# Kernel optimization log

Measured on AMD Instinct MI355X. Metric: run time of the kernel, lower is better.

## Reference

```python
import jax, jax.numpy as jnp
import numpy as np

NE = 32          # n_events
S = 65536        # n_samples
FR = 128         # n_frames
SR = 22050       # samplerate
NRES = 1024      # n_resonances
IEXP = 8         # instr_expressivity
NEXP = 4         # noise_expressivity
NFILT = 64       # n_noise_filters
FSAMP = 512      # noise_filter_samples
NDEF = 64        # n_deformations
NNDEF = 32       # noise_deformations
NENV = 64        # n_envelopes
NDEC = 64        # n_decays
ENV_SMALL = 128  # Envelopes n_samples
ENV_FULL = 8192  # Envelopes full_size
NVERB = 16       # number of impulse responses


def interp_last(x, size):
    # linear interpolation along last axis (align_corners=True style)
    n = x.shape[-1]
    pos = jnp.linspace(0.0, n - 1.0, size)
    lo = jnp.floor(pos).astype(jnp.int32)
    hi = jnp.clip(lo + 1, 0, n - 1)
    w = (pos - lo).astype(x.dtype)
    return x[..., lo] * (1.0 - w) + x[..., hi] * w


def fft_convolve(a, b):
    # linear convolution via zero-padded FFT, keep first n samples
    n = a.shape[-1]
    A = jnp.fft.rfft(a, n=2 * n)
    B = jnp.fft.rfft(b, n=2 * n)
    return jnp.fft.irfft(A * B, n=2 * n)[..., :n]


def select_items(sel, items):
    # softmax-weighted soft lookup over item bank
    return jax.nn.softmax(sel, axis=-1) @ items


def make_waves(n_samples, n_res, sr):
    freqs = np.linspace(20.0, 4000.0, num=n_res // 4)
    t = np.arange(n_samples, dtype=np.float64) / sr
    ph = freqs[:, None] * t[None, :]               # cycles
    sine = np.sin(2 * np.pi * ph)
    saw = 2.0 * (ph % 1.0) - 1.0
    square = np.sign(sine)
    tri = 2.0 * np.abs(saw) - 1.0
    w = np.concatenate([sine, saw, square, tri], axis=0)  # (n_res, n_samples)
    return jnp.asarray(w, dtype=jnp.float32)


def setup_inputs() -> dict:
    key = jax.random.key(0)
    ks = jax.random.split(key, 16)
    u = lambda k, shp: jax.random.uniform(k, shp, minval=-0.02, maxval=0.02, dtype=jnp.float32)
    inp = {
        'res_sel': jax.random.normal(ks[0], (1, NE, IEXP, NRES), jnp.float32),
        'noise_sel': jax.random.normal(ks[1], (1, NE, NEXP, NFILT), jnp.float32),
        'env_sel': jax.random.normal(ks[2], (1, NE, NENV), jnp.float32),
        'dec_sel': jax.random.normal(ks[3], (1, NE, 1, NDEC), jnp.float32),
        'def_sel': jax.random.normal(ks[4], (1, NE, NDEF), jnp.float32),
        'noise_def_sel': jax.random.normal(ks[5], (1, NE, NNDEF), jnp.float32),
        'mix_sel': jax.random.normal(ks[6], (1, NE, 2), jnp.float32),
        'room_sel': jax.random.normal(ks[7], (1, NE, NVERB), jnp.float32),
        'amp': jax.random.uniform(ks[8], (1, NE, 1), dtype=jnp.float32),
        # learned item banks (uniform(-0.02, 0.02) init as in Lookup)
        'r_items': u(ks[9], (NRES, NRES)),
        'n_items': u(ks[10], (NFILT, FSAMP)),
        'e_items': u(ks[11], (NENV, ENV_SMALL)),
        'd_items': u(ks[12], (NDEC, 1)),
        'warp_items': u(ks[13], (NDEF, IEXP * FR)),
        'nwarp_items': u(ks[14], (NNDEF, NEXP * FR)),
        # fixed buffers
        'verbs': jax.random.normal(ks[15], (NVERB, S), jnp.float32) * 0.01,
        'waves': make_waves(S, NRES, SR),
    }
    return inp


def reference(res_sel, noise_sel, env_sel, dec_sel, def_sel, noise_def_sel,
              mix_sel, room_sel, amp, r_items, n_items, e_items, d_items,
              warp_items, nwarp_items, verbs, waves):
    # --- Envelopes: items**2, soft lookup, upsample, multiply by noise, pad ---
    env = select_items(env_sel, e_items ** 2)            # (1, NE, 128)
    env = interp_last(env, ENV_FULL)                     # (1, NE, 8192)
    noise = jax.random.uniform(jax.random.key(42), env.shape,
                               minval=-1.0, maxval=1.0, dtype=env.dtype)
    env = env * noise
    impulses = jnp.pad(env, ((0, 0), (0, 0), (0, S - ENV_FULL)))  # (1, NE, S)

    # --- SampleLookup (windowed noise filters) ---
    k = jnp.arange(FSAMP, dtype=jnp.float32)
    hamming = 0.54 - 0.46 * jnp.cos(2.0 * jnp.pi * k / (FSAMP - 1))
    nfil = select_items(noise_sel, n_items * hamming)    # (1, NE, NEXP, FSAMP)
    nfil = jnp.pad(nfil, ((0, 0), (0, 0), (0, 0), (0, S - FSAMP)))
    filt = fft_convolve(impulses[:, :, None, :], nfil)   # (1, NE, NEXP, S)

    # --- noise Deformations: softmax over channel dim, upsample ---
    nd = select_items(noise_def_sel, nwarp_items)        # (1, NE, NEXP*FR)
    nd = nd.reshape(1, NE, NEXP, FR)
    nd = jax.nn.softmax(nd, axis=2)
    nd = interp_last(nd, S)                              # (1, NE, NEXP, S)
    filtered = (filt * nd).sum(axis=2)                   # (1, NE, S)

    # --- WavetableLookup resonances ---
    res = select_items(res_sel, r_items) @ waves         # (1, NE, IEXP, S)

    # --- Decays: log-domain cumsum -> exponential envelopes ---
    d_pre = 0.5 + jax.nn.sigmoid(d_items) * 0.5          # base_resonance=0.5
    d = select_items(dec_sel, d_pre)                     # (1, NE, 1, 1)
    d = jnp.tile(d, (1, 1, 1, FR))                       # (1, NE, 1, FR)
    d = jnp.exp(jnp.cumsum(jnp.log(d + 1e-12), axis=-1))
    d = interp_last(d, S)                                # (1, NE, 1, S)

    # --- instrument Deformations ---
    w = select_items(def_sel, warp_items)                # (1, NE, IEXP*FR)
    w = w.reshape(1, NE, IEXP, FR)
    w = jax.nn.softmax(w, axis=2)
    w = interp_last(w, S)                                # (1, NE, IEXP, S)

    dres = (res * d * w).sum(axis=2)                     # (1, NE, S)

    # --- excite resonances with filtered noise, add reverb, mix ---
    conv = fft_convolve(filtered, dres)                  # (1, NE, S)
    rooms = select_items(room_sel, verbs)                # (1, NE, S)
    wet = fft_convolve(conv, rooms)
    m = jax.nn.softmax(mix_sel, axis=-1)                 # (1, NE, 2)
    mixed = m[..., 0:1] * conv + m[..., 1:2] * wet
    return mixed * (amp ** 2)                            # (1, NE, S)
```

## Files before the change

kernel.cpp:

```cpp
#include <hip/hip_runtime.h>
#include <math.h>

#define NEV    32
#define NS     65536
#define NFFT   131072
#define ENVS   128
#define ENVF   8192
#define FSAMP2 512
#define NEXP2  4
#define FLEN   8704
#define GD     5622750u
#define GDH    2811375u

enum : size_t {
  O_ENV_SMALL = 0,
  O_NFIL      = 4096,
  O_IMP       = 69632,
  O_ND        = 331776,
  O_WSM       = 348160,
  O_DSM       = 380928,
  O_SCAL      = 385024,
  O_RHO       = 385152,
  O_P1        = 385664,
  O_P2        = 647808,
  O_FILT      = 909952,
  O_DRES      = 1188480,
  O_CONV      = 3285632,
  O_ROOMS     = 5382784,
  O_SWE       = 7479936,
  O_SWN       = 7482048,
  O_SWD       = 7490304,
  O_SWND      = 7492416,
  O_X         = 7742080,
  O_Y         = 16130688,
  O_END       = 24519296,
};

typedef float f32x4 __attribute__((ext_vector_type(4)));
typedef short bf16x8 __attribute__((ext_vector_type(8)));

union U8 { uint4 q; bf16x8 v; unsigned short u[8]; };

__device__ __forceinline__ int imin(int a, int b){ return a < b ? a : b; }

__device__ __forceinline__ float wsum(float v){
  #pragma unroll
  for (int o = 32; o > 0; o >>= 1) v += __shfl_xor(v, o);
  return v;
}
__device__ __forceinline__ float wmax(float v){
  #pragma unroll
  for (int o = 32; o > 0; o >>= 1) v = fmaxf(v, __shfl_xor(v, o));
  return v;
}

__device__ __forceinline__ unsigned short f2bf(float f){
  unsigned u = __float_as_uint(f);
  unsigned r = (u + 0x7fffu + ((u >> 16) & 1u)) >> 16;
  return (unsigned short)r;
}

__device__ __forceinline__ float2 twid(float frac){
  float c, s;
  asm("v_cos_f32 %0, %1" : "=v"(c) : "v"(frac));
  asm("v_sin_f32 %0, %1" : "=v"(s) : "v"(frac));
  return make_float2(c, -s);
}

__device__ __forceinline__ unsigned tf_rotl(unsigned x, int d){ return (x << d) | (x >> (32 - d)); }

__device__ unsigned threefry_bits(unsigned chi, unsigned clo){
  const unsigned k0 = 0u, k1 = 42u, k2 = 0x1BD11BDAu ^ 0u ^ 42u;
  unsigned x0 = chi + k0;
  unsigned x1 = clo + k1;
  x0 += x1; x1 = tf_rotl(x1,13); x1 ^= x0;
  x0 += x1; x1 = tf_rotl(x1,15); x1 ^= x0;
  x0 += x1; x1 = tf_rotl(x1,26); x1 ^= x0;
  x0 += x1; x1 = tf_rotl(x1, 6); x1 ^= x0;
  x0 += k1; x1 += k2 + 1u;
  x0 += x1; x1 = tf_rotl(x1,17); x1 ^= x0;
  x0 += x1; x1 = tf_rotl(x1,29); x1 ^= x0;
  x0 += x1; x1 = tf_rotl(x1,16); x1 ^= x0;
  x0 += x1; x1 = tf_rotl(x1,24); x1 ^= x0;
  x0 += k2; x1 += k0 + 2u;
  x0 += x1; x1 = tf_rotl(x1,13); x1 ^= x0;
  x0 += x1; x1 = tf_rotl(x1,15); x1 ^= x0;
  x0 += x1; x1 = tf_rotl(x1,26); x1 ^= x0;
  x0 += x1; x1 = tf_rotl(x1, 6); x1 ^= x0;
  x0 += k0; x1 += k1 + 3u;
  x0 += x1; x1 = tf_rotl(x1,17); x1 ^= x0;
  x0 += x1; x1 = tf_rotl(x1,29); x1 ^= x0;
  x0 += x1; x1 = tf_rotl(x1,16); x1 ^= x0;
  x0 += x1; x1 = tf_rotl(x1,24); x1 ^= x0;
  x0 += k1; x1 += k2 + 4u;
  x0 += x1; x1 = tf_rotl(x1,13); x1 ^= x0;
  x0 += x1; x1 = tf_rotl(x1,15); x1 ^= x0;
  x0 += x1; x1 = tf_rotl(x1,26); x1 ^= x0;
  x0 += x1; x1 = tf_rotl(x1, 6); x1 ^= x0;
  x0 += k2; x1 += k0 + 5u;
  return x0 ^ x1;
}

__global__ __launch_bounds__(64) void weights_kernel(
    const float* __restrict__ noise_sel, const float* __restrict__ env_sel,
    const float* __restrict__ dec_sel,   const float* __restrict__ def_sel,
    const float* __restrict__ ndef_sel,  const float* __restrict__ mix_sel,
    const float* __restrict__ room_sel,  const float* __restrict__ amp,
    const float* __restrict__ d_items,
    float* __restrict__ swE, float* __restrict__ swN,
    float* __restrict__ swD, float* __restrict__ swND,
    float* __restrict__ d_small, float* __restrict__ scal,
    float* __restrict__ rho)
{
  const int e = blockIdx.x;
  const int l = threadIdx.x;

  {
    float x = env_sel[e*64 + l];
    float mx = wmax(x);
    float ex = expf(x - mx);
    float sm = wsum(ex);
    swE[e*64 + l] = ex / sm;
  }
  #pragma unroll
  for (int x4 = 0; x4 < NEXP2; x4++){
    float v = noise_sel[(e*NEXP2 + x4)*64 + l];
    float mxv = wmax(v);
    float exv = expf(v - mxv);
    float smv = wsum(exv);
    swN[(e*NEXP2 + x4)*64 + l] = exv / smv;
  }
  {
    float x = def_sel[e*64 + l];
    float mx = wmax(x);
    float ex = expf(x - mx);
    float sm = wsum(ex);
    swD[e*64 + l] = ex / sm;
  }
  {
    float x = (l < 32) ? ndef_sel[e*32 + l] : -1e30f;
    float mx = wmax(x);
    float ex = (l < 32) ? expf(x - mx) : 0.f;
    float sm = wsum(ex);
    if (l < 32) swND[e*32 + l] = ex / sm;
  }
  {
    float x = dec_sel[e*64 + l];
    float mx = wmax(x);
    float ex = expf(x - mx);
    float sm = wsum(ex);
    float wgt = ex / sm;
    float di = d_items[l];
    float dp = 0.5f + 0.5f*(1.0f/(1.0f + expf(-di)));
    float d0 = wsum(wgt*dp);
    float ld = logf(d0 + 1e-12f);
    #pragma unroll
    for (int c = 0; c < 2; c++){
      int f = l + 64*c;
      d_small[e*128 + f] = expf((float)(f+1)*ld);
    }
  }
  if (l == 0){
    float a = mix_sel[e*2 + 0], b = mix_sel[e*2 + 1];
    float mm = fmaxf(a, b);
    float ea = expf(a - mm), eb = expf(b - mm);
    float ss = ea + eb;
    scal[e*4 + 0] = ea/ss;
    scal[e*4 + 1] = eb/ss;
    float am = amp[e];
    scal[e*4 + 2] = am*am;
  }
  {
    float x = (l < 16) ? room_sel[e*16 + l] : -1e30f;
    float mx = wmax(x);
    float ex = (l < 16) ? expf(x - mx) : 0.f;
    float sm = wsum(ex);
    if (l < 16) rho[e*16 + l] = ex/sm;
  }
}

__global__ __launch_bounds__(128) void envs_kernel(
    const float* __restrict__ swE, const float* __restrict__ e_items,
    float* __restrict__ env_small)
{
  const int e = blockIdx.x, j = threadIdx.x;
  __shared__ float sw[64];
  if (j < 64) sw[j] = swE[e*64 + j];
  __syncthreads();
  float acc = 0.f;
  #pragma unroll 8
  for (int k = 0; k < 64; k++){ float it = e_items[k*ENVS + j]; acc += sw[k]*(it*it); }
  env_small[e*ENVS + j] = acc;
}

__global__ __launch_bounds__(256) void nfil_kernel(
    const float* __restrict__ swN, const float* __restrict__ n_items,
    float* __restrict__ nfil)
{
  const int b = blockIdx.x;
  const int tid = threadIdx.x;
  __shared__ float sw[64];
  if (tid < 64) sw[tid] = swN[b*64 + tid];
  __syncthreads();
  #pragma unroll
  for (int c = 0; c < 2; c++){
    int tau = tid + 256*c;
    float acc = 0.f;
    #pragma unroll 8
    for (int f = 0; f < 64; f++) acc += sw[f]*n_items[f*FSAMP2 + tau];
    float ham = 0.54f - 0.46f*cosf((6.2831853071795864769f * (float)tau) / 511.0f);
    nfil[b*FSAMP2 + tau] = acc*ham;
  }
}

__global__ __launch_bounds__(128) void warp_kernel(
    const float* __restrict__ swD, const float* __restrict__ warp_items,
    float* __restrict__ w_small)
{
  const int e = blockIdx.x, f = threadIdx.x;
  __shared__ float sw[64];
  if (f < 64) sw[f] = swD[e*64 + f];
  __syncthreads();
  float acc[8] = {0,0,0,0,0,0,0,0};
  for (int k = 0; k < 64; k++){
    float wk = sw[k];
    const float* row = warp_items + (size_t)k*1024 + f;
    #pragma unroll
    for (int i = 0; i < 8; i++) acc[i] += wk*row[i*128];
  }
  float mx = -1e30f;
  #pragma unroll
  for (int i = 0; i < 8; i++) mx = fmaxf(mx, acc[i]);
  float ev[8]; float s = 0.f;
  #pragma unroll
  for (int i = 0; i < 8; i++){ ev[i] = expf(acc[i] - mx); s += ev[i]; }
  #pragma unroll
  for (int i = 0; i < 8; i++) w_small[(e*8 + i)*128 + f] = ev[i]/s;
}

__global__ __launch_bounds__(128) void nwarp_kernel(
    const float* __restrict__ swND, const float* __restrict__ nwarp_items,
    float* __restrict__ nd_small)
{
  const int e = blockIdx.x, f = threadIdx.x;
  __shared__ float sw[32];
  if (f < 32) sw[f] = swND[e*32 + f];
  __syncthreads();
  float acc[4] = {0,0,0,0};
  for (int k = 0; k < 32; k++){
    float wk = sw[k];
    const float* row = nwarp_items + (size_t)k*512 + f;
    #pragma unroll
    for (int x = 0; x < 4; x++) acc[x] += wk*row[x*128];
  }
  float mx = -1e30f;
  #pragma unroll
  for (int x = 0; x < 4; x++) mx = fmaxf(mx, acc[x]);
  float ev[4]; float s = 0.f;
  #pragma unroll
  for (int x = 0; x < 4; x++){ ev[x] = expf(acc[x] - mx); s += ev[x]; }
  #pragma unroll
  for (int x = 0; x < 4; x++) nd_small[(e*4 + x)*128 + f] = ev[x]/s;
}

__global__ __launch_bounds__(64) void prep_kernel(
    const float* __restrict__ noise_sel, const float* __restrict__ env_sel,
    const float* __restrict__ dec_sel,   const float* __restrict__ def_sel,
    const float* __restrict__ ndef_sel,  const float* __restrict__ mix_sel,
    const float* __restrict__ room_sel,  const float* __restrict__ amp,
    const float* __restrict__ n_items,   const float* __restrict__ e_items,
    const float* __restrict__ d_items,   const float* __restrict__ warp_items,
    const float* __restrict__ nwarp_items,
    float* __restrict__ env_small, float* __restrict__ nfil,
    float* __restrict__ nd_small,  float* __restrict__ w_small,
    float* __restrict__ d_small,   float* __restrict__ scal,
    float* __restrict__ rho)
{
  const int e = blockIdx.x;
  const int l = threadIdx.x;
  __shared__ float sw[64];
  __shared__ float buf[1024];

  {
    float x = env_sel[e*64 + l];
    float mx = wmax(x);
    float ex = expf(x - mx);
    float sm = wsum(ex);
    sw[l] = ex / sm;
  }
  __syncthreads();
  #pragma unroll
  for (int c = 0; c < 2; c++){
    int j = l + 64*c;
    float acc = 0.f;
    for (int k = 0; k < 64; k++){ float it = e_items[k*ENVS + j]; acc += sw[k]*(it*it); }
    env_small[e*ENVS + j] = acc;
  }
  __syncthreads();

  for (int x = 0; x < NEXP2; x++){
    float v = noise_sel[(e*NEXP2 + x)*64 + l];
    float mxv = wmax(v);
    float exv = expf(v - mxv);
    float smv = wsum(exv);
    sw[l] = exv / smv;
    __syncthreads();
    for (int c = 0; c < 8; c++){
      int tau = l + 64*c;
      float acc = 0.f;
      for (int f = 0; f < 64; f++) acc += sw[f]*n_items[f*FSAMP2 + tau];
      float ham = 0.54f - 0.46f*cosf((6.2831853071795864769f * (float)tau) / 511.0f);
      nfil[(e*NEXP2 + x)*FSAMP2 + tau] = acc*ham;
    }
    __syncthreads();
  }

  {
    float x = def_sel[e*64 + l];
    float mx = wmax(x);
    float ex = expf(x - mx);
    float sm = wsum(ex);
    sw[l] = ex / sm;
  }
  __syncthreads();
  for (int c = 0; c < 16; c++){
    int idx = l + 64*c;
    float acc = 0.f;
    for (int k = 0; k < 64; k++) acc += sw[k]*warp_items[k*1024 + idx];
    buf[idx] = acc;
  }
  __syncthreads();
  #pragma unroll
  for (int c = 0; c < 2; c++){
    int f = l + 64*c;
    float mx = -1e30f;
    for (int i = 0; i < 8; i++) mx = fmaxf(mx, buf[i*128 + f]);
    float ev[8]; float s = 0.f;
    for (int i = 0; i < 8; i++){ ev[i] = expf(buf[i*128 + f] - mx); s += ev[i]; }
    for (int i = 0; i < 8; i++) w_small[(e*8 + i)*128 + f] = ev[i]/s;
  }
  __syncthreads();

  {
    float x = (l < 32) ? ndef_sel[e*32 + l] : -1e30f;
    float mx = wmax(x);
    float ex = (l < 32) ? expf(x - mx) : 0.f;
    float sm = wsum(ex);
    sw[l] = (l < 32) ? ex/sm : 0.f;
  }
  __syncthreads();
  for (int c = 0; c < 8; c++){
    int idx = l + 64*c;
    float acc = 0.f;
    for (int k = 0; k < 32; k++) acc += sw[k]*nwarp_items[k*512 + idx];
    buf[idx] = acc;
  }
  __syncthreads();
  #pragma unroll
  for (int c = 0; c < 2; c++){
    int j = l + 64*c;
    float mx = -1e30f;
    for (int x = 0; x < 4; x++) mx = fmaxf(mx, buf[x*128 + j]);
    float ev[4]; float s = 0.f;
    for (int x = 0; x < 4; x++){ ev[x] = expf(buf[x*128 + j] - mx); s += ev[x]; }
    for (int x = 0; x < 4; x++) nd_small[(e*4 + x)*128 + j] = ev[x]/s;
  }
  __syncthreads();

  {
    float x = dec_sel[e*64 + l];
    float mx = wmax(x);
    float ex = expf(x - mx);
    float sm = wsum(ex);
    float wgt = ex / sm;
    float di = d_items[l];
    float dp = 0.5f + 0.5f*(1.0f/(1.0f + expf(-di)));
    float d0 = wsum(wgt*dp);
    float ld = logf(d0 + 1e-12f);
    #pragma unroll
    for (int c = 0; c < 2; c++){
      int f = l + 64*c;
      d_small[e*128 + f] = expf((float)(f+1)*ld);
    }
  }
  if (l == 0){
    float a = mix_sel[e*2 + 0], b = mix_sel[e*2 + 1];
    float mm = fmaxf(a, b);
    float ea = expf(a - mm), eb = expf(b - mm);
    float ss = ea + eb;
    scal[e*4 + 0] = ea/ss;
    scal[e*4 + 1] = eb/ss;
    float am = amp[e];
    scal[e*4 + 2] = am*am;
  }
  {
    float x = (l < 16) ? room_sel[e*16 + l] : -1e30f;
    float mx = wmax(x);
    float ex = (l < 16) ? expf(x - mx) : 0.f;
    float sm = wsum(ex);
    if (l < 16) rho[e*16 + l] = ex/sm;
  }
}

__global__ __launch_bounds__(256) void p1_softmax_kernel(
    const float* __restrict__ res_sel, float* __restrict__ P1)
{
  const int m = blockIdx.x;
  const int tid = threadIdx.x;
  __shared__ float red[4], red2[4];
  const float* row = res_sel + (size_t)m*1024;
  float4 v = ((const float4*)row)[tid];
  float mx = fmaxf(fmaxf(v.x, v.y), fmaxf(v.z, v.w));
  #pragma unroll
  for (int o = 32; o > 0; o >>= 1) mx = fmaxf(mx, __shfl_xor(mx, o));
  if ((tid & 63) == 0) red[tid >> 6] = mx;
  __syncthreads();
  mx = fmaxf(fmaxf(red[0], red[1]), fmaxf(red[2], red[3]));
  float e0 = expf(v.x - mx), e1 = expf(v.y - mx), e2 = expf(v.z - mx), e3 = expf(v.w - mx);
  float s = e0 + e1 + e2 + e3;
  #pragma unroll
  for (int o = 32; o > 0; o >>= 1) s += __shfl_xor(s, o);
  if ((tid & 63) == 0) red2[tid >> 6] = s;
  __syncthreads();
  s = red2[0] + red2[1] + red2[2] + red2[3];
  float inv = 1.0f/s;
  ((float4*)(P1 + (size_t)m*1024))[tid] = make_float4(e0*inv, e1*inv, e2*inv, e3*inv);
}

__global__ __launch_bounds__(256) void p2_kernel(
    const float* __restrict__ P1, const float* __restrict__ r_items,
    float* __restrict__ P2)
{
  __shared__ __align__(16) float sp1[8][1024];
  const int bx = blockIdx.x;
  const int mg = blockIdx.y;
  const int tid = threadIdx.x;
  for (int idx = tid; idx < 2048; idx += 256)
    ((float4*)&sp1[0][0])[idx] = ((const float4*)(P1 + (size_t)mg*8*1024))[idx];
  __syncthreads();
  const int n = bx*256 + tid;
  float acc[8] = {0,0,0,0,0,0,0,0};
  for (int k = 0; k < 1024; k++){
    float wv = r_items[(size_t)k*1024 + n];
    #pragma unroll
    for (int r = 0; r < 8; r++) acc[r] += sp1[r][k]*wv;
  }
  #pragma unroll
  for (int r = 0; r < 8; r++) P2[(size_t)(mg*8 + r)*1024 + n] = acc[r];
}

__global__ __launch_bounds__(256) void split_a_kernel(
    const float* __restrict__ P2, unsigned short* __restrict__ Ahi)
{
  const int row = blockIdx.x;
  for (int k = threadIdx.x; k < 1024; k += 256){
    float f = P2[(size_t)row*1024 + k];
    Ahi[(size_t)(k >> 3)*2048 + row*8 + (k & 7)] = f2bf(f);
  }
}

__global__ __launch_bounds__(256) void env_noise_kernel(
    const float* __restrict__ env_small, float* __restrict__ impulses)
{
  const int flat = blockIdx.x*256 + threadIdx.x;
  const int e = flat >> 13, i = flat & 8191;
  unsigned bits = threefry_bits(0u, (unsigned)flat);
  float u01 = __uint_as_float((bits >> 9) | 0x3f800000u) - 1.0f;
  float nz  = fmaxf(-1.0f, u01*2.0f - 1.0f);
  float pos = (float)i * (127.0f/8191.0f);
  int lo = (int)floorf(pos);
  int hi = imin(lo + 1, 127);
  float w = pos - (float)lo;
  const float* es = env_small + e*ENVS;
  float v = es[lo]*(1.0f - w) + es[hi]*w;
  impulses[flat] = v*nz;
}

__global__ __launch_bounds__(256) void filt_kernel(
    const float* __restrict__ nfil, const float* __restrict__ impulses,
    const float* __restrict__ nd_small, float* __restrict__ filtered)
{
  __shared__ float nf[4*512];
  __shared__ float imp[768];
  const int e = blockIdx.y, t0 = blockIdx.x*256, tid = threadIdx.x;
  for (int idx = tid; idx < 2048; idx += 256) nf[idx] = nfil[e*2048 + idx];
  for (int idx = tid; idx < 768; idx += 256){
    int g = t0 - 512 + idx;
    imp[idx] = (g >= 0 && g < ENVF) ? impulses[e*ENVF + g] : 0.f;
  }
  __syncthreads();
  const int t = t0 + tid;
  float s0 = 0.f, s1 = 0.f, s2 = 0.f, s3 = 0.f;
  for (int tau = 0; tau < 512; tau++){
    float iv = imp[512 + tid - tau];
    s0 += nf[0*512 + tau]*iv;
    s1 += nf[1*512 + tau]*iv;
    s2 += nf[2*512 + tau]*iv;
    s3 += nf[3*512 + tau]*iv;
  }
  float pos = (float)t * (127.0f/65535.0f);
  int lo = (int)floorf(pos);
  int hi = imin(lo + 1, 127);
  float w = pos - (float)lo;
  const float* nds = nd_small + e*512;
  float acc = 0.f;
  acc += s0*(nds[0*128 + lo]*(1.0f - w) + nds[0*128 + hi]*w);
  acc += s1*(nds[1*128 + lo]*(1.0f - w) + nds[1*128 + hi]*w);
  acc += s2*(nds[2*128 + lo]*(1.0f - w) + nds[2*128 + hi]*w);
  acc += s3*(nds[3*128 + lo]*(1.0f - w) + nds[3*128 + hi]*w);
  filtered[e*FLEN + t] = acc;
}

__global__ __launch_bounds__(256) void rooms_kernel(
    const float* __restrict__ verbs, const float* __restrict__ rho,
    float* __restrict__ rooms)
{
  const int t = blockIdx.x*256 + threadIdx.x;
  const int e = blockIdx.y;
  float acc = 0.f;
  #pragma unroll
  for (int v = 0; v < 16; v++) acc += rho[e*16 + v]*verbs[(size_t)v*NS + t];
  rooms[(size_t)e*NS + t] = acc;
}

__device__ __noinline__ float slow_wave(int wf, int n, int i){
  const double stp = 3980.0 / 255.0;
  double fi = (i == 255) ? 4000.0 : __dadd_rn(__dmul_rn((double)i, stp), 20.0);
  double tn = (double)n / 22050.0;
  double ph = __dmul_rn(fi, tn);
  double fr = ph - trunc(ph);
  if (wf == 1) return (float)(2.0*fr - 1.0);
  if (wf == 3){ double sw = 2.0*fr - 1.0; return (float)(2.0*fabs(sw) - 1.0); }
  if (fr == 0.0 || fr == 0.5){
    if (ph == 0.0) return 0.0f;
    double sv = sin(__dmul_rn(6.283185307179586, ph));
    return (sv > 0.0) ? 1.0f : ((sv < 0.0) ? -1.0f : 0.0f);
  }
  return (fr < 0.5) ? 1.0f : -1.0f;
}

__device__ __forceinline__ void gen8(int wf, int n, int i0,
                                     unsigned m_in, unsigned stepn,
                                     U8& bh, U8& bl)
{
  unsigned m = m_in;
  #pragma unroll
  for (int j = 0; j < 8; j++){
    float fr = (float)m * (1.0f/5622750.0f);
    float val;
    bool rare;
    if (wf == 0){
      asm("v_sin_f32 %0, %1" : "=v"(val) : "v"(fr));
      rare = false;
    } else if (wf == 1){
      val = fmaf(fr, 2.0f, -1.0f);
      rare = (m == 0u);
    } else if (wf == 2){
      val = (m < GDH) ? 1.0f : -1.0f;
      rare = (m == 0u) || (m == GDH);
    } else {
      val = fmaf(fabsf(fmaf(fr, 2.0f, -1.0f)), 2.0f, -1.0f);
      rare = (m == 0u);
    }
    if (rare) val = slow_wave(wf, n, i0 + j);
    unsigned ub = __float_as_uint(val);
    unsigned th = ub & 0xFFFF0000u;
    float lres = val - __uint_as_float(th);
    bh.u[j] = (unsigned short)(ub >> 16);
    bl.u[j] = (unsigned short)(__float_as_uint(lres) >> 16);
    m += stepn;
    if (m >= GD) m -= GD;
  }
}

__global__ __launch_bounds__(512, 2) void gemm_dres_gen3_kernel(
    const unsigned short* __restrict__ Ahi,
    const float* __restrict__ w_small, const float* __restrict__ d_small,
    float* __restrict__ dres)
{
  __shared__ __align__(16) unsigned short Abuf[2][8192];

  const int tid = threadIdx.x;
  const int l = tid & 63, w = tid >> 6;
  const int g = l >> 4, c = l & 15;
  const int n = blockIdx.x*128 + w*16 + c;

  f32x4 acc[16];
  #pragma unroll
  for (int m = 0; m < 16; m++) acc[m] = (f32x4){0.f,0.f,0.f,0.f};

  const unsigned stepn = (3980u*(unsigned)n) % GD;
  const unsigned s32 = (32u*stepn) % GD;
  const unsigned K0g = 3980u*(unsigned)(g*8) + 5100u;
  const unsigned m0 = (unsigned)(((unsigned long long)(unsigned)n * K0g) % GD);
  unsigned mseg = m0;

  typedef const __attribute__((address_space(1))) void GV;
  typedef __attribute__((address_space(3))) void LV;

  #pragma unroll
  for (int q = 0; q < 2; q++){
    const unsigned short* src = Ahi + (size_t)q*4096 + (size_t)w*512 + (size_t)l*8;
    __builtin_amdgcn_global_load_lds((GV*)src, (LV*)&Abuf[0][q*4096 + w*512], 16, 0, 0);
  }
  __syncthreads();

  for (int k0 = 0; k0 < 1024; k0 += 32){
    const int cur = (k0 >> 5) & 1, nxt = cur ^ 1;
    const int wf = k0 >> 8;
    if ((k0 & 255) == 0) mseg = m0;

    if (k0 + 32 < 1024){
      const size_t slice = (size_t)((k0 + 32) >> 5) * 8192;
      #pragma unroll
      for (int q = 0; q < 2; q++){
        const unsigned short* src = Ahi + slice + (size_t)q*4096 + (size_t)w*512 + (size_t)l*8;
        __builtin_amdgcn_global_load_lds((GV*)src, (LV*)&Abuf[nxt][q*4096 + w*512], 16, 0, 0);
      }
    }

    const int i0 = (k0 & 255) + g*8;
    U8 bh, bl;
    gen8(wf, n, i0, mseg, stepn, bh, bl);
    mseg += s32; if (mseg >= GD) mseg -= GD;

    #pragma unroll
    for (int m = 0; m < 16; m++){
      U8 ah;
      ah.q = *(const uint4*)&Abuf[cur][g*2048 + (m*16 + c)*8];
      acc[m] = __builtin_amdgcn_mfma_f32_16x16x32_bf16(ah.v, bh.v, acc[m], 0, 0, 0);
      acc[m] = __builtin_amdgcn_mfma_f32_16x16x32_bf16(ah.v, bl.v, acc[m], 0, 0, 0);
    }
    __syncthreads();
  }

  const int t = n;
  float pos = (float)t * (127.0f/65535.0f);
  int lo = (int)floorf(pos);
  int hi = imin(lo + 1, 127);
  float fr = pos - (float)lo;
  #pragma unroll
  for (int m = 0; m < 16; m++){
    int e = 2*m + (g >> 1);
    float s = 0.f;
    #pragma unroll
    for (int jj = 0; jj < 4; jj++){
      int i = (g & 1)*4 + jj;
      const float* wr = w_small + (size_t)(e*8 + i)*128;
      float wi = wr[lo]*(1.0f - fr) + wr[hi]*fr;
      s += wi * acc[m][jj];
    }
    s += __shfl_xor(s, 16);
    if ((g & 1) == 0){
      float de = d_small[e*128 + lo]*(1.0f - fr) + d_small[e*128 + hi]*fr;
      dres[(size_t)e*NS + t] = de * s;
    }
  }
}

__global__ __launch_bounds__(256) void gemm_dres_kernel(
    const float* __restrict__ P2, const float* __restrict__ waves,
    const float* __restrict__ w_small, const float* __restrict__ d_small,
    float* __restrict__ dres)
{
  __shared__ __align__(16) float At[32][256];
  __shared__ __align__(16) float Bt[32][64];
  const int tid = threadIdx.x;
  const int tx = tid & 15, ty = tid >> 4;
  const int n0 = blockIdx.x * 64;
  float acc[16][4];
  #pragma unroll
  for (int a = 0; a < 16; a++)
    #pragma unroll
    for (int b = 0; b < 4; b++) acc[a][b] = 0.f;

  for (int k0 = 0; k0 < 1024; k0 += 32){
    {
      const float4* src = (const float4*)(P2 + (size_t)tid*1024 + k0);
      #pragma unroll
      for (int q = 0; q < 8; q++){
        float4 v = src[q];
        At[q*4 + 0][tid] = v.x; At[q*4 + 1][tid] = v.y;
        At[q*4 + 2][tid] = v.z; At[q*4 + 3][tid] = v.w;
      }
    }
    {
      int c  = tid & 15;
      int kr = tid >> 4;
      *(float4*)&Bt[kr][c*4]      = *((const float4*)(waves + (size_t)(k0 + kr)*NS + n0) + c);
      *(float4*)&Bt[kr + 16][c*4] = *((const float4*)(waves + (size_t)(k0 + kr + 16)*NS + n0) + c);
    }
    __syncthreads();
    #pragma unroll 4
    for (int k = 0; k < 32; k++){
      float a[16];
      *(float4*)&a[0]  = *(const float4*)&At[k][ty*16 + 0];
      *(float4*)&a[4]  = *(const float4*)&At[k][ty*16 + 4];
      *(float4*)&a[8]  = *(const float4*)&At[k][ty*16 + 8];
      *(float4*)&a[12] = *(const float4*)&At[k][ty*16 + 12];
      float4 b = *(const float4*)&Bt[k][tx*4];
      #pragma unroll
      for (int mi = 0; mi < 16; mi++){
        acc[mi][0] += a[mi]*b.x;
        acc[mi][1] += a[mi]*b.y;
        acc[mi][2] += a[mi]*b.z;
        acc[mi][3] += a[mi]*b.w;
      }
    }
    __syncthreads();
  }

  #pragma unroll
  for (int ni = 0; ni < 4; ni++){
    int t = n0 + tx*4 + ni;
    float pos = (float)t * (127.0f/65535.0f);
    int lo = (int)floorf(pos);
    int hi = imin(lo + 1, 127);
    float w = pos - (float)lo;
    #pragma unroll
    for (int ev2 = 0; ev2 < 2; ev2++){
      int e = ty*2 + ev2;
      float de = d_small[e*128 + lo]*(1.0f - w) + d_small[e*128 + hi]*w;
      float s = 0.f;
      #pragma unroll
      for (int i = 0; i < 8; i++){
        const float* wrow = w_small + (size_t)(e*8 + i)*128;
        float wi = wrow[lo]*(1.0f - w) + wrow[hi]*w;
        s += wi * acc[ev2*8 + i][ni];
      }
      dres[(size_t)e*NS + t] = de * s;
    }
  }
}


template<int L, int LOG2L, int DIR>
__device__ __forceinline__ void fft_core(float*& ra, float*& ia, float*& rb, float*& ib)
{
  __shared__ float2 stw[256];
  const int tid = threadIdx.x;
  stw[tid] = twid((float)tid * (1.0f/512.0f));
  #pragma unroll
  for (int s = 0; s < LOG2L; s++){
    const int Ns = 1 << s;
    __syncthreads();
    #pragma unroll
    for (int q = 0; q < 8; q++){
      int bf = tid + 256*q;
      int r  = bf >> (LOG2L - 1);
      int j  = bf & (L/2 - 1);
      int sw = (r & 7) << 2;
      int jm = j & (Ns - 1);
      float2 w = stw[jm << (8 - s)];
      float wi = (DIR > 0) ? w.y : -w.y;
      float a_re = ra[r*L + (j ^ sw)];
      float a_im = ia[r*L + (j ^ sw)];
      float b_re = ra[r*L + ((j + L/2) ^ sw)];
      float b_im = ia[r*L + ((j + L/2) ^ sw)];
      float t_re = b_re*w.x - b_im*wi;
      float t_im = b_re*wi + b_im*w.x;
      int d = ((j >> s) << (s + 1)) | jm;
      rb[r*L + (d ^ sw)]        = a_re + t_re;
      ib[r*L + (d ^ sw)]        = a_im + t_im;
      rb[r*L + ((d + Ns) ^ sw)] = a_re - t_re;
      ib[r*L + ((d + Ns) ^ sw)] = a_im - t_im;
    }
    float* t;
    t = ra; ra = rb; rb = t;
    t = ia; ia = ib; ib = t;
  }
  __syncthreads();
}

__global__ __launch_bounds__(256) void fwd512_pack_kernel(
    const float* __restrict__ srcA, int lenA, int strideA,
    const float* __restrict__ srcB, int lenB, int strideB,
    float2* __restrict__ Bt)
{
  __shared__ float reA[4096], imA[4096], reB[4096], imB[4096];
  const int e = blockIdx.y, t1 = blockIdx.x*8, tid = threadIdx.x;
  #pragma unroll
  for (int q = 0; q < 4; q++){
    int flat = tid + 256*q;
    int n2 = flat >> 1;
    int rb = (flat & 1)*4;
    int nb = t1 + rb + 256*n2;
    float4 va = make_float4(0.f,0.f,0.f,0.f);
    float4 vb = make_float4(0.f,0.f,0.f,0.f);
    if (nb < lenA) va = *(const float4*)(srcA + (size_t)e*strideA + nb);
    if (nb < lenB) vb = *(const float4*)(srcB + (size_t)e*strideB + nb);
    #pragma unroll
    for (int j = 0; j < 4; j++){
      int r = rb + j;
      int sw = (r & 7) << 2;
      reA[r*512 + (n2 ^ sw)] = (&va.x)[j];
      imA[r*512 + (n2 ^ sw)] = (&vb.x)[j];
    }
  }
  float *ra = reA, *ia = imA, *rb2 = reB, *ib2 = imB;
  fft_core<512, 9, +1>(ra, ia, rb2, ib2);
  float2* dst = Bt + ((size_t)e << 17);
  #pragma unroll
  for (int q = 0; q < 16; q++){
    int idx = tid + 256*q;
    int r = idx & 7, k2 = idx >> 3;
    int n1 = t1 + r;
    int sw = (r & 7) << 2;
    float xr = ra[r*512 + (k2 ^ sw)];
    float xi = ia[r*512 + (k2 ^ sw)];
    float2 w = twid((float)(n1*k2) * (1.0f/131072.0f));
    dst[k2*256 + n1] = make_float2(xr*w.x - xi*w.y, xr*w.y + xi*w.x);
  }
}

__global__ __launch_bounds__(256) void fwd512_pack_rooms_kernel(
    const float* __restrict__ verbs, const float* __restrict__ rho,
    float2* __restrict__ Bt)
{
  __shared__ float reA[4096], imA[4096], reB[4096], imB[4096];
  __shared__ float srho[32];
  const int e = blockIdx.y, t1 = blockIdx.x*8, tid = threadIdx.x;
  if (tid < 32) srho[tid] = rho[(2*e)*16 + tid];
  __syncthreads();
  #pragma unroll
  for (int q = 0; q < 4; q++){
    int flat = tid + 256*q;
    int n2 = flat >> 1;
    int rb = (flat & 1)*4;
    int nb = t1 + rb + 256*n2;
    float4 va = make_float4(0.f,0.f,0.f,0.f);
    float4 vb = make_float4(0.f,0.f,0.f,0.f);
    if (nb < NS){
      #pragma unroll
      for (int v = 0; v < 16; v++){
        float4 w4 = *(const float4*)(verbs + (size_t)v*NS + nb);
        float r0 = srho[v], r1 = srho[16 + v];
        va.x += r0*w4.x; va.y += r0*w4.y; va.z += r0*w4.z; va.w += r0*w4.w;
        vb.x += r1*w4.x; vb.y += r1*w4.y; vb.z += r1*w4.z; vb.w += r1*w4.w;
      }
    }
    #pragma unroll
    for (int j = 0; j < 4; j++){
      int r = rb + j;
      int sw = (r & 7) << 2;
      reA[r*512 + (n2 ^ sw)] = (&va.x)[j];
      imA[r*512 + (n2 ^ sw)] = (&vb.x)[j];
    }
  }
  float *ra = reA, *ia = imA, *rb2 = reB, *ib2 = imB;
  fft_core<512, 9, +1>(ra, ia, rb2, ib2);
  float2* dst = Bt + ((size_t)e << 17);
  #pragma unroll
  for (int q = 0; q < 16; q++){
    int idx = tid + 256*q;
    int r = idx & 7, k2 = idx >> 3;
    int n1 = t1 + r;
    int sw = (r & 7) << 2;
    float xr = ra[r*512 + (k2 ^ sw)];
    float xi = ia[r*512 + (k2 ^ sw)];
    float2 w = twid((float)(n1*k2) * (1.0f/131072.0f));
    dst[k2*256 + n1] = make_float2(xr*w.x - xi*w.y, xr*w.y + xi*w.x);
  }
}

__global__ __launch_bounds__(256) void fwd256_kernel(float2* __restrict__ S)
{
  __shared__ float reA[4096], imA[4096], reB[4096], imB[4096];
  const int e = blockIdx.y, K0 = blockIdx.x*16, tid = threadIdx.x;
  float2* base = S + ((size_t)e << 17) + (size_t)K0*256;
  #pragma unroll
  for (int q = 0; q < 16; q++){
    int idx = tid + 256*q;
    int r = idx >> 8, col = idx & 255;
    float2 v = base[r*256 + col];
    int sw = (r & 7) << 2;
    reA[r*256 + (col ^ sw)] = v.x;
    imA[r*256 + (col ^ sw)] = v.y;
  }
  float *ra = reA, *ia = imA, *rb = reB, *ib = imB;
  fft_core<256, 8, +1>(ra, ia, rb, ib);
  #pragma unroll
  for (int q = 0; q < 16; q++){
    int idx = tid + 256*q;
    int r = idx >> 8, col = idx & 255;
    int sw = (r & 7) << 2;
    base[r*256 + col] = make_float2(ra[r*256 + (col ^ sw)], ia[r*256 + (col ^ sw)]);
  }
}

__global__ __launch_bounds__(256) void inv256_mul2_kernel(
    const float2* __restrict__ ZA, const float2* __restrict__ ZB,
    float2* __restrict__ Ut)
{
  __shared__ float reA[4096], imA[4096], reB[4096], imB[4096];
  const int e = blockIdx.y, K0 = blockIdx.x*16, tid = threadIdx.x;
  const float2* Za = ZA + ((size_t)e << 17);
  const float2* Zb = ZB + ((size_t)e << 17);
  #pragma unroll
  for (int q = 0; q < 16; q++){
    int idx = tid + 256*q;
    int r = idx >> 8, col = idx & 255;
    int k2 = K0 + r;
    int k2p, k1p;
    if (k2 == 0){ k2p = 0; k1p = (256 - col) & 255; }
    else        { k2p = 512 - k2; k1p = 255 - col; }
    float2 za  = Za[(size_t)k2*256 + col];
    float2 zap = Za[(size_t)k2p*256 + k1p];
    float2 zb  = Zb[(size_t)k2*256 + col];
    float2 zbp = Zb[(size_t)k2p*256 + k1p];
    float a0r = 0.5f*(za.x + zap.x), a0i = 0.5f*(za.y - zap.y);
    float a1r = 0.5f*(za.y + zap.y), a1i = 0.5f*(zap.x - za.x);
    float b0r = 0.5f*(zb.x + zbp.x), b0i = 0.5f*(zb.y - zbp.y);
    float b1r = 0.5f*(zb.y + zbp.y), b1i = 0.5f*(zbp.x - zb.x);
    float p0r = a0r*b0r - a0i*b0i, p0i = a0r*b0i + a0i*b0r;
    float p1r = a1r*b1r - a1i*b1i, p1i = a1r*b1i + a1i*b1r;
    int sw = (r & 7) << 2;
    reA[r*256 + (col ^ sw)] = p0r - p1i;
    imA[r*256 + (col ^ sw)] = p0i + p1r;
  }
  float *ra = reA, *ia = imA, *rb = reB, *ib = imB;
  fft_core<256, 8, -1>(ra, ia, rb, ib);
  float2* dst = Ut + ((size_t)e << 17);
  #pragma unroll
  for (int q = 0; q < 16; q++){
    int idx = tid + 256*q;
    int r = idx & 15, n1 = idx >> 4;
    int k2 = K0 + r;
    int sw = (r & 7) << 2;
    float xr = ra[r*256 + (n1 ^ sw)];
    float xi = ia[r*256 + (n1 ^ sw)];
    float2 w = twid((float)(n1*k2) * (1.0f/131072.0f));
    dst[n1*512 + k2] = make_float2(xr*w.x + xi*w.y, xi*w.x - xr*w.y);
  }
}

__global__ __launch_bounds__(256) void inv512_fwdpack2_kernel(
    const float2* __restrict__ Ut, float* __restrict__ conv,
    float2* __restrict__ Bt)
{
  __shared__ float reA[4096], imA[4096], reB[4096], imB[4096];
  const int e = blockIdx.y, t1 = blockIdx.x*8, tid = threadIdx.x;
  const float2* base = Ut + ((size_t)e << 17) + (size_t)t1*512;
  #pragma unroll
  for (int q = 0; q < 16; q++){
    int idx = tid + 256*q;
    int r = idx >> 9, col = idx & 511;
    float2 v = base[r*512 + col];
    int sw = (r & 7) << 2;
    reA[r*512 + (col ^ sw)] = v.x;
    imA[r*512 + (col ^ sw)] = v.y;
  }
  float *ra = reA, *ia = imA, *rb = reB, *ib = imB;
  fft_core<512, 9, -1>(ra, ia, rb, ib);
  const float s = 1.0f/131072.0f;
  #pragma unroll
  for (int q = 0; q < 16; q++){
    int idx = tid + 256*q;
    int r = idx & 7, n2 = idx >> 3;
    int sw = (r & 7) << 2;
    int pos = r*512 + (n2 ^ sw);
    if (n2 < 256){
      int n = (t1 + r) + 256*n2;
      float y0 = ra[pos]*s, y1 = ia[pos]*s;
      conv[(size_t)(2*e)*NS + n]     = y0;
      conv[(size_t)(2*e + 1)*NS + n] = y1;
      rb[pos] = y0; ib[pos] = y1;
    } else {
      rb[pos] = 0.f; ib[pos] = 0.f;
    }
  }
  __syncthreads();
  float *r2 = rb, *i2 = ib, *r3 = ra, *i3 = ia;
  fft_core<512, 9, +1>(r2, i2, r3, i3);
  float2* dst = Bt + ((size_t)e << 17);
  #pragma unroll
  for (int q = 0; q < 16; q++){
    int idx = tid + 256*q;
    int r = idx & 7, k2 = idx >> 3;
    int n1 = t1 + r;
    int sw = (r & 7) << 2;
    float xr = r2[r*512 + (k2 ^ sw)];
    float xi = i2[r*512 + (k2 ^ sw)];
    float2 w = twid((float)(n1*k2) * (1.0f/131072.0f));
    dst[k2*256 + n1] = make_float2(xr*w.x - xi*w.y, xr*w.y + xi*w.x);
  }
}

__global__ __launch_bounds__(256) void inv512_mix2_kernel(
    const float2* __restrict__ Ut, const float* __restrict__ conv,
    const float* __restrict__ scal, float* __restrict__ dst)
{
  __shared__ float reA[4096], imA[4096], reB[4096], imB[4096];
  const int e = blockIdx.y, t1 = blockIdx.x*8, tid = threadIdx.x;
  const float2* base = Ut + ((size_t)e << 17) + (size_t)t1*512;
  #pragma unroll
  for (int q = 0; q < 16; q++){
    int idx = tid + 256*q;
    int r = idx >> 9, col = idx & 511;
    float2 v = base[r*512 + col];
    int sw = (r & 7) << 2;
    reA[r*512 + (col ^ sw)] = v.x;
    imA[r*512 + (col ^ sw)] = v.y;
  }
  float *ra = reA, *ia = imA, *rb = reB, *ib = imB;
  fft_core<512, 9, -1>(ra, ia, rb, ib);
  const float s = 1.0f/131072.0f;
  const int e0 = 2*e, e1 = 2*e + 1;
  float m00 = scal[e0*4 + 0], m10 = scal[e0*4 + 1], a20 = scal[e0*4 + 2];
  float m01 = scal[e1*4 + 0], m11 = scal[e1*4 + 1], a21 = scal[e1*4 + 2];
  #pragma unroll
  for (int q = 0; q < 8; q++){
    int idx = tid + 256*q;
    int r = idx & 7, n2 = idx >> 3;
    int n = (t1 + r) + 256*n2;
    int sw = (r & 7) << 2;
    int pos = r*512 + (n2 ^ sw);
    float w0 = ra[pos]*s, w1 = ia[pos]*s;
    size_t g0 = (size_t)e0*NS + n, g1 = (size_t)e1*NS + n;
    dst[g0] = (m00*conv[g0] + m10*w0)*a20;
    dst[g1] = (m01*conv[g1] + m11*w1)*a21;
  }
}

template<int MODE>
__global__ __launch_bounds__(256) void tconv_kernel(
    const float* __restrict__ sig, int sig_len, int sig_stride,
    const float* __restrict__ go, const float* __restrict__ scal,
    float* __restrict__ dst)
{
  __shared__ __align__(16) float cs[2048];
  __shared__ __align__(16) float rs[4104];
  const int e = blockIdx.y;
  const int t0 = blockIdx.x * 2048;
  const int tid = threadIdx.x;
  const int tb = tid * 8;
  float acc[8] = {0,0,0,0,0,0,0,0};
  const int kcap = imin(sig_len, t0 + 2048);
  for (int c0 = 0; c0 < kcap; c0 += 2048){
    __syncthreads();
    for (int idx = tid; idx < 2048; idx += 256){
      int gsi = c0 + idx;
      cs[idx] = (gsi < sig_len) ? sig[(size_t)e*sig_stride + gsi] : 0.f;
    }
    const int rb = t0 - c0 - 2056;
    for (int idx = tid; idx < 4104; idx += 256){
      int g = rb + idx;
      rs[idx] = (g >= 0 && g < NS) ? go[(size_t)e*NS + g] : 0.f;
    }
    __syncthreads();
    float W[12];
    int P = tb + 2056;
    *(float4*)&W[0] = *(const float4*)&rs[P - 4];
    *(float4*)&W[4] = *(const float4*)&rs[P];
    *(float4*)&W[8] = *(const float4*)&rs[P + 4];
    for (int u = 0; u < 512; u++){
      float4 f4 = *(const float4*)&cs[4*u];
      #pragma unroll
      for (int j = 0; j < 8; j++){
        acc[j] += f4.x*W[4 + j];
        acc[j] += f4.y*W[3 + j];
        acc[j] += f4.z*W[2 + j];
        acc[j] += f4.w*W[1 + j];
      }
      #pragma unroll
      for (int x2 = 11; x2 >= 4; x2--) W[x2] = W[x2 - 4];
      P -= 4;
      *(float4*)&W[0] = *(const float4*)&rs[P - 4];
    }
  }
  if (MODE == 0){
    #pragma unroll
    for (int j = 0; j < 8; j++) dst[(size_t)e*NS + t0 + tb + j] = acc[j];
  } else {
    float m0 = scal[e*4 + 0], m1 = scal[e*4 + 1], a2 = scal[e*4 + 2];
    #pragma unroll
    for (int j = 0; j < 8; j++){
      size_t gi = (size_t)e*NS + t0 + tb + j;
      dst[gi] = (m0*sig[gi] + m1*acc[j]) * a2;
    }
  }
}

extern "C" void kernel_launch(void* const* d_in, const int* in_sizes, int n_in,
                              void* d_out, int out_size, void* d_ws, size_t ws_size,
                              hipStream_t stream)
{
  (void)in_sizes; (void)n_in; (void)out_size;
  const float* res_sel     = (const float*)d_in[0];
  const float* noise_sel   = (const float*)d_in[1];
  const float* env_sel     = (const float*)d_in[2];
  const float* dec_sel     = (const float*)d_in[3];
  const float* def_sel     = (const float*)d_in[4];
  const float* ndef_sel    = (const float*)d_in[5];
  const float* mix_sel     = (const float*)d_in[6];
  const float* room_sel    = (const float*)d_in[7];
  const float* amp         = (const float*)d_in[8];
  const float* r_items     = (const float*)d_in[9];
  const float* n_items     = (const float*)d_in[10];
  const float* e_items     = (const float*)d_in[11];
  const float* d_items     = (const float*)d_in[12];
  const float* warp_items  = (const float*)d_in[13];
  const float* nwarp_items = (const float*)d_in[14];
  const float* verbs       = (const float*)d_in[15];
  const float* waves       = (const float*)d_in[16];
  float* ws  = (float*)d_ws;
  float* out = (float*)d_out;

  const bool big_ws = ws_size >= (size_t)O_END * sizeof(float);

  if (big_ws) {
    weights_kernel<<<dim3(NEV), dim3(64), 0, stream>>>(
        noise_sel, env_sel, dec_sel, def_sel, ndef_sel, mix_sel, room_sel, amp,
        d_items, ws + O_SWE, ws + O_SWN, ws + O_SWD, ws + O_SWND,
        ws + O_DSM, ws + O_SCAL, ws + O_RHO);
    envs_kernel<<<dim3(NEV), dim3(128), 0, stream>>>(ws + O_SWE, e_items, ws + O_ENV_SMALL);
    nfil_kernel<<<dim3(128), dim3(256), 0, stream>>>(ws + O_SWN, n_items, ws + O_NFIL);
    warp_kernel<<<dim3(NEV), dim3(128), 0, stream>>>(ws + O_SWD, warp_items, ws + O_WSM);
    nwarp_kernel<<<dim3(NEV), dim3(128), 0, stream>>>(ws + O_SWND, nwarp_items, ws + O_ND);

    p1_softmax_kernel<<<dim3(256), dim3(256), 0, stream>>>(res_sel, ws + O_P1);
    p2_kernel<<<dim3(4, 32), dim3(256), 0, stream>>>(ws + O_P1, r_items, ws + O_P2);

    env_noise_kernel<<<dim3(1024), dim3(256), 0, stream>>>(ws + O_ENV_SMALL, ws + O_IMP);
    filt_kernel<<<dim3(34, NEV), dim3(256), 0, stream>>>(ws + O_NFIL, ws + O_IMP, ws + O_ND, ws + O_FILT);

    unsigned short* Ahi = (unsigned short*)(ws + O_X);
    split_a_kernel<<<dim3(256), dim3(256), 0, stream>>>(ws + O_P2, Ahi);
    gemm_dres_gen3_kernel<<<dim3(512), dim3(512), 0, stream>>>(
        Ahi, ws + O_WSM, ws + O_DSM, ws + O_DRES);

    float2* Xf = (float2*)(ws + O_X);
    float2* Xd = (float2*)(ws + O_X + 4194304);
    float2* Xr = (float2*)(ws + O_Y);
    float2* Uc = (float2*)(ws + O_Y + 4194304);
    float2* Xc = Xf;
    float2* Uw = Xd;

    fwd512_pack_kernel<<<dim3(32, 16), dim3(256), 0, stream>>>(
        ws + O_FILT, FLEN, 2*FLEN, ws + O_FILT + FLEN, FLEN, 2*FLEN, Xf);
    fwd256_kernel<<<dim3(32, 16), dim3(256), 0, stream>>>(Xf);
    fwd512_pack_kernel<<<dim3(32, 16), dim3(256), 0, stream>>>(
        ws + O_DRES, NS, 2*NS, ws + O_DRES + NS, NS, 2*NS, Xd);
    fwd256_kernel<<<dim3(32, 16), dim3(256), 0, stream>>>(Xd);
    fwd512_pack_rooms_kernel<<<dim3(32, 16), dim3(256), 0, stream>>>(
        verbs, ws + O_RHO, Xr);
    fwd256_kernel<<<dim3(32, 16), dim3(256), 0, stream>>>(Xr);

    inv256_mul2_kernel<<<dim3(32, 16), dim3(256), 0, stream>>>(Xf, Xd, Uc);
    inv512_fwdpack2_kernel<<<dim3(32, 16), dim3(256), 0, stream>>>(Uc, ws + O_CONV, Xc);
    fwd256_kernel<<<dim3(32, 16), dim3(256), 0, stream>>>(Xc);
    inv256_mul2_kernel<<<dim3(32, 16), dim3(256), 0, stream>>>(Xc, Xr, Uw);
    inv512_mix2_kernel<<<dim3(32, 16), dim3(256), 0, stream>>>(
        Uw, ws + O_CONV, ws + O_SCAL, out);
  } else {
    prep_kernel<<<dim3(NEV), dim3(64), 0, stream>>>(
        noise_sel, env_sel, dec_sel, def_sel, ndef_sel, mix_sel, room_sel, amp,
        n_items, e_items, d_items, warp_items, nwarp_items,
        ws + O_ENV_SMALL, ws + O_NFIL, ws + O_ND, ws + O_WSM,
        ws + O_DSM, ws + O_SCAL, ws + O_RHO);
    p1_softmax_kernel<<<dim3(256), dim3(256), 0, stream>>>(res_sel, ws + O_P1);
    p2_kernel<<<dim3(4, 32), dim3(256), 0, stream>>>(ws + O_P1, r_items, ws + O_P2);
    env_noise_kernel<<<dim3(1024), dim3(256), 0, stream>>>(ws + O_ENV_SMALL, ws + O_IMP);
    filt_kernel<<<dim3(34, NEV), dim3(256), 0, stream>>>(ws + O_NFIL, ws + O_IMP, ws + O_ND, ws + O_FILT);
    rooms_kernel<<<dim3(256, NEV), dim3(256), 0, stream>>>(verbs, ws + O_RHO, ws + O_ROOMS);
    gemm_dres_kernel<<<dim3(1024), dim3(256), 0, stream>>>(
        ws + O_P2, waves, ws + O_WSM, ws + O_DSM, ws + O_DRES);
    tconv_kernel<0><<<dim3(32, NEV), dim3(256), 0, stream>>>(
        ws + O_FILT, FLEN, FLEN, ws + O_DRES, (const float*)nullptr, ws + O_CONV);
    tconv_kernel<1><<<dim3(32, NEV), dim3(256), 0, stream>>>(
        ws + O_CONV, NS, NS, ws + O_ROOMS, ws + O_SCAL, out);
  }
}
```

Before: 413.4 us.

## Replace radix-2 shared-memory FFT stages with radix-4 butterflies

Replaces the radix-2 Stockham FFT core used by all the 512- and 256-point passes with a radix-4 version (one radix-2 stage plus four radix-4 stages for L=512, four radix-4 stages for L=256). This roughly halves the number of LDS read/write passes and __syncthreads barriers per FFT. Twiddles are now computed per butterfly via twid() plus complex squaring instead of a shared lookup table, which adds ALU work and slight rounding differences.

Result: faster. 388.2 us (-6.1%).

```diff
diff --git a/kernel.cpp b/kernel.cpp
--- a/kernel.cpp
+++ b/kernel.cpp
@@ -734,40 +734,89 @@
 }
 
 
-template<int L, int LOG2L, int DIR>
-__device__ __forceinline__ void fft_core(float*& ra, float*& ia, float*& rb, float*& ib)
-{
-  __shared__ float2 stw[256];
+template<int L, int Ns, int DIR>
+__device__ __forceinline__ void r4_stage(const float* __restrict__ xr,
+                                         const float* __restrict__ xi,
+                                         float* __restrict__ yr,
+                                         float* __restrict__ yi)
+{
   const int tid = threadIdx.x;
-  stw[tid] = twid((float)tid * (1.0f/512.0f));
-  #pragma unroll
-  for (int s = 0; s < LOG2L; s++){
-    const int Ns = 1 << s;
+  constexpr int BPR = L/4;
+  #pragma unroll
+  for (int q = 0; q < 4; q++){
+    int bf = tid + 256*q;
+    int r  = bf / BPR;
+    int j  = bf % BPR;
+    int sw = (r & 7) << 2;
+    int jm = j & (Ns - 1);
+    float2 w1 = twid((float)jm * (1.0f/(4.0f*(float)Ns)));
+    if (DIR < 0) w1.y = -w1.y;
+    float2 w2 = make_float2(w1.x*w1.x - w1.y*w1.y, 2.0f*w1.x*w1.y);
+    float2 w3 = make_float2(w2.x*w1.x - w2.y*w1.y, w2.x*w1.y + w2.y*w1.x);
+    const float* xrr = xr + r*L;
+    const float* xir = xi + r*L;
+    float ar  = xrr[j ^ sw],           ai  = xir[j ^ sw];
+    float b0r = xrr[(j+BPR) ^ sw],     b0i = xir[(j+BPR) ^ sw];
+    float c0r = xrr[(j+2*BPR) ^ sw],   c0i = xir[(j+2*BPR) ^ sw];
+    float d0r = xrr[(j+3*BPR) ^ sw],   d0i = xir[(j+3*BPR) ^ sw];
+    float br = b0r*w1.x - b0i*w1.y,  bi = b0r*w1.y + b0i*w1.x;
+    float cr = c0r*w2.x - c0i*w2.y,  ci = c0r*w2.y + c0i*w2.x;
+    float dr = d0r*w3.x - d0i*w3.y,  di = d0r*w3.y + d0i*w3.x;
+    float apc_r = ar + cr, apc_i = ai + ci;
+    float amc_r = ar - cr, amc_i = ai - ci;
+    float bpd_r = br + dr, bpd_i = bi + di;
+    float bmd_r = br - dr, bmd_i = bi - di;
+    int dbase = ((j - jm) << 2) + jm;
+    float* yrr = yr + r*L;
+    float* yir = yi + r*L;
+    yrr[dbase ^ sw]          = apc_r + bpd_r;
+    yir[dbase ^ sw]          = apc_i + bpd_i;
+    yrr[(dbase + 2*Ns) ^ sw] = apc_r - bpd_r;
+    yir[(dbase + 2*Ns) ^ sw] = apc_i - bpd_i;
+    if (DIR > 0){
+      yrr[(dbase + Ns) ^ sw]   = amc_r + bmd_i;
+      yir[(dbase + Ns) ^ sw]   = amc_i - bmd_r;
+      yrr[(dbase + 3*Ns) ^ sw] = amc_r - bmd_i;
+      yir[(dbase + 3*Ns) ^ sw] = amc_i + bmd_r;
+    } else {
+      yrr[(dbase + Ns) ^ sw]   = amc_r - bmd_i;
+      yir[(dbase + Ns) ^ sw]   = amc_i + bmd_r;
+      yrr[(dbase + 3*Ns) ^ sw] = amc_r + bmd_i;
+      yir[(dbase + 3*Ns) ^ sw] = amc_i - bmd_r;
+    }
+  }
+}
+
+#define FFT_SWAP { float* t_; t_=ra;ra=rb;rb=t_; t_=ia;ia=ib;ib=t_; }
+
+template<int L, int DIR>
+__device__ __forceinline__ void fft_core4(float*& ra, float*& ia, float*& rb, float*& ib)
+{
+  const int tid = threadIdx.x;
+  if (L == 512){
     __syncthreads();
     #pragma unroll
     for (int q = 0; q < 8; q++){
       int bf = tid + 256*q;
-      int r  = bf >> (LOG2L - 1);
-      int j  = bf & (L/2 - 1);
+      int r = bf >> 8, j = bf & 255;
       int sw = (r & 7) << 2;
-      int jm = j & (Ns - 1);
-      float2 w = stw[jm << (8 - s)];
-      float wi = (DIR > 0) ? w.y : -w.y;
-      float a_re = ra[r*L + (j ^ sw)];
-      float a_im = ia[r*L + (j ^ sw)];
-      float b_re = ra[r*L + ((j + L/2) ^ sw)];
-      float b_im = ia[r*L + ((j + L/2) ^ sw)];
-      float t_re = b_re*w.x - b_im*wi;
-      float t_im = b_re*wi + b_im*w.x;
-      int d = ((j >> s) << (s + 1)) | jm;
-      rb[r*L + (d ^ sw)]        = a_re + t_re;
-      ib[r*L + (d ^ sw)]        = a_im + t_im;
-      rb[r*L + ((d + Ns) ^ sw)] = a_re - t_re;
-      ib[r*L + ((d + Ns) ^ sw)] = a_im - t_im;
-    }
-    float* t;
-    t = ra; ra = rb; rb = t;
-    t = ia; ia = ib; ib = t;
+      float ar = ra[r*512 + (j ^ sw)],        ai = ia[r*512 + (j ^ sw)];
+      float br = ra[r*512 + ((j+256) ^ sw)],  bi = ia[r*512 + ((j+256) ^ sw)];
+      rb[r*512 + ((2*j) ^ sw)]   = ar + br;
+      ib[r*512 + ((2*j) ^ sw)]   = ai + bi;
+      rb[r*512 + ((2*j+1) ^ sw)] = ar - br;
+      ib[r*512 + ((2*j+1) ^ sw)] = ai - bi;
+    }
+    FFT_SWAP
+    __syncthreads(); r4_stage<512,   2, DIR>(ra, ia, rb, ib); FFT_SWAP
+    __syncthreads(); r4_stage<512,   8, DIR>(ra, ia, rb, ib); FFT_SWAP
+    __syncthreads(); r4_stage<512,  32, DIR>(ra, ia, rb, ib); FFT_SWAP
+    __syncthreads(); r4_stage<512, 128, DIR>(ra, ia, rb, ib); FFT_SWAP
+  } else {
+    __syncthreads(); r4_stage<256,   1, DIR>(ra, ia, rb, ib); FFT_SWAP
+    __syncthreads(); r4_stage<256,   4, DIR>(ra, ia, rb, ib); FFT_SWAP
+    __syncthreads(); r4_stage<256,  16, DIR>(ra, ia, rb, ib); FFT_SWAP
+    __syncthreads(); r4_stage<256,  64, DIR>(ra, ia, rb, ib); FFT_SWAP
   }
   __syncthreads();
 }
@@ -798,7 +847,7 @@
     }
   }
   float *ra = reA, *ia = imA, *rb2 = reB, *ib2 = imB;
-  fft_core<512, 9, +1>(ra, ia, rb2, ib2);
+  fft_core4<512, +1>(ra, ia, rb2, ib2);
   float2* dst = Bt + ((size_t)e << 17);
   #pragma unroll
   for (int q = 0; q < 16; q++){
@@ -848,7 +897,7 @@
     }
   }
   float *ra = reA, *ia = imA, *rb2 = reB, *ib2 = imB;
-  fft_core<512, 9, +1>(ra, ia, rb2, ib2);
+  fft_core4<512, +1>(ra, ia, rb2, ib2);
   float2* dst = Bt + ((size_t)e << 17);
   #pragma unroll
   for (int q = 0; q < 16; q++){
@@ -878,7 +927,7 @@
     imA[r*256 + (col ^ sw)] = v.y;
   }
   float *ra = reA, *ia = imA, *rb = reB, *ib = imB;
-  fft_core<256, 8, +1>(ra, ia, rb, ib);
+  fft_core4<256, +1>(ra, ia, rb, ib);
   #pragma unroll
   for (int q = 0; q < 16; q++){
     int idx = tid + 256*q;
@@ -919,7 +968,7 @@
     imA[r*256 + (col ^ sw)] = p0i + p1r;
   }
   float *ra = reA, *ia = imA, *rb = reB, *ib = imB;
-  fft_core<256, 8, -1>(ra, ia, rb, ib);
+  fft_core4<256, -1>(ra, ia, rb, ib);
   float2* dst = Ut + ((size_t)e << 17);
   #pragma unroll
   for (int q = 0; q < 16; q++){
@@ -951,7 +1000,7 @@
     imA[r*512 + (col ^ sw)] = v.y;
   }
   float *ra = reA, *ia = imA, *rb = reB, *ib = imB;
-  fft_core<512, 9, -1>(ra, ia, rb, ib);
+  fft_core4<512, -1>(ra, ia, rb, ib);
   const float s = 1.0f/131072.0f;
   #pragma unroll
   for (int q = 0; q < 16; q++){
@@ -971,7 +1020,7 @@
   }
   __syncthreads();
   float *r2 = rb, *i2 = ib, *r3 = ra, *i3 = ia;
-  fft_core<512, 9, +1>(r2, i2, r3, i3);
+  fft_core4<512, +1>(r2, i2, r3, i3);
   float2* dst = Bt + ((size_t)e << 17);
   #pragma unroll
   for (int q = 0; q < 16; q++){
@@ -1003,7 +1052,7 @@
     imA[r*512 + (col ^ sw)] = v.y;
   }
   float *ra = reA, *ia = imA, *rb = reB, *ib = imB;
-  fft_core<512, 9, -1>(ra, ia, rb, ib);
+  fft_core4<512, -1>(ra, ia, rb, ib);
   const float s = 1.0f/131072.0f;
   const int e0 = 2*e, e1 = 2*e + 1;
   float m00 = scal[e0*4 + 0], m10 = scal[e0*4 + 1], a20 = scal[e0*4 + 2];
```
